# Performance work log

Measured on AMD Instinct MI355X. Metric: run time of the kernel, lower is better.

Reference implementation:

```python
import jax, jax.numpy as jnp
import numpy as np
from jax import lax

EPS = 1e-5
K = 32  # k_neighbor

def conv1(x, w):
    # x: [B, Cin, L], w: [Cout, Cin] (1x1 conv, no bias)
    return jnp.einsum('bcl,oc->bol', x, w)

def bn(x, g, b):
    # BatchNorm1d in training mode: batch statistics over (batch, length)
    m = jnp.mean(x, axis=(0, 2), keepdims=True)
    v = jnp.var(x, axis=(0, 2), keepdims=True)
    return g[None, :, None] * (x - m) / jnp.sqrt(v + EPS) + b[None, :, None]

def res_block(x, w1, g1, b1, w2, g2, b2):
    h = jax.nn.gelu(bn(conv1(x, w1), g1, b1), approximate=False)
    h = bn(conv1(h, w2), g2, b2)
    return jax.nn.gelu(h + x, approximate=False)

def extraction(x, conv_w, bn_g, bn_b, fw, fg, fb):
    # conv_w: [n_blocks, 2, C, C]; bn_g/bn_b: [n_blocks, 2, C]
    for i in range(conv_w.shape[0]):
        x = res_block(x, conv_w[i, 0], bn_g[i, 0], bn_b[i, 0],
                      conv_w[i, 1], bn_g[i, 1], bn_b[i, 1])
    # TransformerBlock: ffn (conv+BN) with residual + GELU
    return jax.nn.gelu(x + bn(conv1(x, fw), fg, fb), approximate=False)

def setup_inputs() -> dict:
    key = jax.random.key(0)
    ks = jax.random.split(key, 16)
    B, N, S, C = 8, 4096, 1024, 128  # C = out_channel = 2*channel
    inp = {
        'xyz': jax.random.normal(ks[0], (B, N, 3), dtype=jnp.float32),
        'x': jax.random.normal(ks[1], (B, 64, N), dtype=jnp.float32),
        'fps_idx': jax.random.randint(ks[2], (B, S), 0, N, dtype=jnp.int64),
        'pre_conv_w': jax.random.normal(ks[3], (2, 2, C, C), dtype=jnp.float32) * 0.05,
        'pre_bn_g': jnp.ones((2, 2, C), jnp.float32),
        'pre_bn_b': jnp.zeros((2, 2, C), jnp.float32),
        'pre_ffn_w': jax.random.normal(ks[4], (C, C), dtype=jnp.float32) * 0.05,
        'pre_ffn_g': jnp.ones((C,), jnp.float32),
        'pre_ffn_b': jnp.zeros((C,), jnp.float32),
        'pos_conv_w': jax.random.normal(ks[5], (2, 2, C, C), dtype=jnp.float32) * 0.05,
        'pos_bn_g': jnp.ones((2, 2, C), jnp.float32),
        'pos_bn_b': jnp.zeros((2, 2, C), jnp.float32),
        'pos_ffn_w': jax.random.normal(ks[6], (C, C), dtype=jnp.float32) * 0.05,
        'pos_ffn_g': jnp.ones((C,), jnp.float32),
        'pos_ffn_b': jnp.zeros((C,), jnp.float32),
    }
    return inp

def reference(xyz, x, fps_idx,
              pre_conv_w, pre_bn_g, pre_bn_b, pre_ffn_w, pre_ffn_g, pre_ffn_b,
              pos_conv_w, pos_bn_g, pos_bn_b, pos_ffn_w, pos_ffn_g, pos_ffn_b):
    B, N, _ = xyz.shape
    S = fps_idx.shape[1]
    points = jnp.swapaxes(x, 1, 2)  # [B, N, d]
    d = points.shape[-1]

    # --- LocalGrouper ---
    new_xyz = jnp.take_along_axis(xyz, fps_idx[:, :, None], axis=1)      # [B, S, 3]
    new_pts = jnp.take_along_axis(points, fps_idx[:, :, None], axis=1)  # [B, S, d]

    # squared distances [B, S, N]
    sqr = (jnp.sum(new_xyz ** 2, -1)[:, :, None]
           + jnp.sum(xyz ** 2, -1)[:, None, :]
           - 2.0 * jnp.einsum('bsc,bnc->bsn', new_xyz, xyz))
    idx = lax.top_k(-sqr, K)[1]  # [B, S, K] smallest distances

    grouped = jnp.take_along_axis(points, idx.reshape(B, S * K)[:, :, None],
                                  axis=1).reshape(B, S, K, d)
    center = new_pts[:, :, None, :]  # [B, S, 1, d]
    feat = jnp.concatenate([grouped - center,
                            jnp.broadcast_to(center, grouped.shape)], axis=-1)  # [B,S,K,2d]

    C = 2 * d
    # --- PreExtraction: [B,S,K,C] -> [B*S, C, K] -> maxpool -> [B, C, S] ---
    y = jnp.swapaxes(feat, 2, 3).reshape(B * S, C, K)
    y = extraction(y, pre_conv_w, pre_bn_g, pre_bn_b, pre_ffn_w, pre_ffn_g, pre_ffn_b)
    y = jnp.max(y, axis=-1).reshape(B, S, C)
    y = jnp.swapaxes(y, 1, 2)  # [B, C, S]

    # --- PosExtraction ---
    y = extraction(y, pos_conv_w, pos_bn_g, pos_bn_b, pos_ffn_w, pos_ffn_g, pos_ffn_b)
    return (new_xyz, y)
```

## Files before the change

kernel.cpp:

```cpp
#include <hip/hip_runtime.h>
#include <math.h>

typedef unsigned short ushort_t;
typedef unsigned long long u64;
typedef unsigned int uint32;

#define B_ 8
#define N_ 4096
#define S_ 1024
#define K_ 32
#define C_ 128
#define NCOL1 (B_*S_*K_)
#define NCOL2 (B_*S_)
#define EPS_ 1e-5f

typedef ushort_t us8 __attribute__((ext_vector_type(8)));
typedef short s16x8 __attribute__((ext_vector_type(8)));
typedef float f32x4 __attribute__((ext_vector_type(4)));

__device__ __forceinline__ float bf2f(ushort_t u){ return __uint_as_float(((uint32)u)<<16); }
__device__ __forceinline__ ushort_t f2bf(float f){
    uint32 x = __float_as_uint(f);
    return (ushort_t)((x + 0x7FFFu + ((x>>16)&1u)) >> 16);
}
__device__ __forceinline__ float gelu_f(float v){
    float az = fabsf(v)*0.70710678118654752f;
    float t  = __builtin_amdgcn_rcpf(fmaf(0.3275911f, az, 1.0f));
    float p  = fmaf(fmaf(fmaf(fmaf(1.061405429f, t, -1.453152027f), t, 1.421413741f), t,
                   -0.284496736f), t, 0.254829592f)*t;
    float e  = __expf(-az*az);
    float er = fmaf(-p, e, 1.0f);
    float s  = (v < 0.0f) ? -er : er;
    return 0.5f*v*(1.0f+s);
}
__device__ __forceinline__ u64 shfl_xor_u64(u64 v, int m){
    int lo = __shfl_xor((int)(v & 0xFFFFFFFFull), m, 64);
    int hi = __shfl_xor((int)(v >> 32), m, 64);
    return (((u64)(uint32)hi) << 32) | (uint32)lo;
}
__device__ __forceinline__ void gl_lds16(const char* gp, char* lp){
    __builtin_amdgcn_global_load_lds((const __attribute__((address_space(1))) void*)gp,
                                     (__attribute__((address_space(3))) void*)lp, 16, 0, 0);
}

__global__ __launch_bounds__(256) void transpose_kernel(const float* __restrict__ x, float* __restrict__ xT){
    __shared__ float t[64][65];
    int b  = blockIdx.x >> 6;
    int n0 = (blockIdx.x & 63) * 64;
    int tx = threadIdx.x & 63, ty = threadIdx.x >> 6;
    #pragma unroll
    for (int i=0;i<16;i++){
        int c = i*4 + ty;
        t[c][tx] = x[((long)(b*64 + c))*N_ + n0 + tx];
    }
    __syncthreads();
    #pragma unroll
    for (int i=0;i<16;i++){
        int n = i*4 + ty;
        xT[((long)(b*N_ + n0 + n))*64 + tx] = t[tx][n];
    }
}

__global__ __launch_bounds__(256) void knn_kernel(const float* __restrict__ xyz, const int* __restrict__ fps,
                                                  int* __restrict__ idxg, float* __restrict__ newxyz){
    __shared__ uint32 hist[4096];
    __shared__ u64    cand[1024];
    __shared__ u64    out_keys[64];
    __shared__ uint32 csum[256];
    __shared__ uint32 wtot[4];
    __shared__ uint32 shv[8];
    __shared__ u64    wred[4];
    __shared__ u64    winner;

    int tid = threadIdx.x;
    int wv = tid >> 6, l = tid & 63;
    int bs = blockIdx.x;
    int b  = bs >> 10;
    int qi = fps[bs];
    const float* qb = xyz + ((long)b*N_ + qi)*3;
    float qx = qb[0], qy = qb[1], qz = qb[2];
    if (tid < 3) newxyz[(long)bs*3 + tid] = qb[tid];
    const float* xb = xyz + (long)b*N_*3;

    for (int i=tid;i<1024;i+=256) hist[i]=0;
    if (tid < 8) shv[tid]=0;
    __syncthreads();

    uint32 dbits[16];
    #pragma unroll
    for (int i=0;i<16;i++){
        int n = i*256 + tid;
        float dx = xb[n*3+0]-qx, dy = xb[n*3+1]-qy, dz = xb[n*3+2]-qz;
        float d = dx*dx + dy*dy + dz*dz;
        dbits[i] = __float_as_uint(d);
        atomicAdd(&hist[dbits[i]>>21], 1u);
    }
    __syncthreads();

    {
        uint32 h4[4]; uint32 csumv=0;
        #pragma unroll
        for (int i=0;i<4;i++){ h4[i]=hist[tid*4+i]; csumv+=h4[i]; }
        uint32 sc = csumv;
        #pragma unroll
        for (int off=1; off<64; off<<=1){ uint32 o=__shfl_up(sc,off,64); if (l>=off) sc+=o; }
        if (l==63) wtot[wv]=sc;
        csum[tid]=sc;
        __syncthreads();
        uint32 base=0;
        for (int w2=0; w2<wv; w2++) base += wtot[w2];
        uint32 cum = base + csum[tid] - csumv;
        #pragma unroll
        for (int i=0;i<4;i++){
            if (cum <= 31u && 31u < cum + h4[i]){ shv[0]=(uint32)(tid*4+i); shv[1]=cum; }
            cum += h4[i];
        }
    }
    __syncthreads();
    uint32 b1 = shv[0], cl1 = shv[1];

    for (int i=tid;i<4096;i+=256) hist[i]=0;
    __syncthreads();
    #pragma unroll
    for (int i=0;i<16;i++){
        uint32 u = dbits[i];
        if ((u>>21)==b1) atomicAdd(&hist[(u>>9)&0xFFFu], 1u);
    }
    __syncthreads();

    uint32 r2 = 31u - cl1;
    {
        uint32 h[16]; uint32 csumv=0;
        #pragma unroll
        for (int i=0;i<16;i++){ h[i]=hist[tid*16+i]; csumv += h[i]; }
        uint32 sc = csumv;
        #pragma unroll
        for (int off=1; off<64; off<<=1){ uint32 o=__shfl_up(sc,off,64); if (l>=off) sc+=o; }
        if (l==63) wtot[wv]=sc;
        csum[tid]=sc;
        __syncthreads();
        uint32 base=0;
        for (int w2=0; w2<wv; w2++) base += wtot[w2];
        uint32 cum = base + csum[tid] - csumv;
        #pragma unroll
        for (int i=0;i<16;i++){
            if (cum <= r2 && r2 < cum + h[i]){ shv[2]=(uint32)(tid*16+i); shv[3]=cum; }
            cum += h[i];
        }
    }
    __syncthreads();
    uint32 b2 = shv[2], cl2 = shv[3];
    uint32 nless = cl1 + cl2;

    #pragma unroll
    for (int i=0;i<16;i++){
        uint32 u = dbits[i];
        int n = i*256 + tid;
        uint32 bb1 = u >> 21;
        if (bb1 > b1) continue;
        u64 key = (((u64)u)<<32) | (uint32)n;
        if (bb1 < b1){
            uint32 p = atomicAdd(&shv[4],1u); out_keys[p] = key;
        } else {
            uint32 bb2 = (u>>9)&0xFFFu;
            if (bb2 < b2){ uint32 p = atomicAdd(&shv[4],1u); out_keys[p] = key; }
            else if (bb2 == b2){ uint32 p = atomicAdd(&shv[5],1u); if (p < 1024u) cand[p] = key; }
        }
    }
    __syncthreads();

    if (shv[5] > 1024u){
        uint32 alive = 0xFFFFu;
        for (int r=0;r<K_;r++){
            u64 lmin = ~0ull;
            #pragma unroll
            for (int i=0;i<16;i++){
                u64 k = (((u64)dbits[i])<<32) | (uint32)(i*256+tid);
                if (((alive>>i)&1u) && k < lmin) lmin = k;
            }
            #pragma unroll
            for (int off=32; off>=1; off>>=1){
                u64 o = shfl_xor_u64(lmin, off);
                if (o < lmin) lmin = o;
            }
            if (l == 0) wred[wv] = lmin;
            __syncthreads();
            if (tid == 0){
                u64 m = wred[0];
                if (wred[1]<m) m=wred[1];
                if (wred[2]<m) m=wred[2];
                if (wred[3]<m) m=wred[3];
                winner = m;
                idxg[(long)bs*K_ + r] = (int)(m & 0xFFFFFFFFull);
            }
            __syncthreads();
            u64 w = winner;
            #pragma unroll
            for (int i=0;i<16;i++){
                u64 k = (((u64)dbits[i])<<32) | (uint32)(i*256+tid);
                if (k == w) alive &= ~(1u<<i);
            }
        }
    } else if (wv == 0){
        uint32 cb   = shv[5];
        uint32 need = 32u - nless;
        for (uint32 r=0; r<need; r++){
            u64 lmin = ~0ull;
            for (uint32 s=l; s<cb; s+=64){ u64 kk = cand[s]; if (kk < lmin) lmin = kk; }
            #pragma unroll
            for (int off=32; off>=1; off>>=1){
                u64 o = shfl_xor_u64(lmin, off);
                if (o < lmin) lmin = o;
            }
            for (uint32 s=l; s<cb; s+=64){ if (cand[s]==lmin) cand[s] = ~0ull; }
            if (l==0) out_keys[nless + r] = lmin;
        }
        u64 key = (l < 32) ? out_keys[l] : ~0ull;
        #pragma unroll
        for (uint32 k=2; k<=64; k<<=1){
            bool dir = ((l & k)==0);
            #pragma unroll
            for (uint32 j=k>>1; j>=1; j>>=1){
                u64 o = shfl_xor_u64(key, j);
                bool lower = ((l & j)==0);
                u64 mn = (key < o) ? key : o;
                u64 mx = (key < o) ? o : key;
                key = (lower == dir) ? mn : mx;
            }
        }
        if (l < 32) idxg[(long)bs*K_ + l] = (int)(key & 0xFFFFFFFFull);
    }
}

__global__ __launch_bounds__(256) void build_kernel(const float* __restrict__ xT, const int* __restrict__ fps,
                                                    const int* __restrict__ idxg, ushort_t* __restrict__ A){
    long col = (long)blockIdx.x*256 + threadIdx.x;
    long bs  = col >> 5;
    int  b   = (int)(bs >> 10);
    int  n   = idxg[col];
    int  cn  = fps[bs];
    const float4* pr = (const float4*)(xT + ((long)b*N_ + n )*64);
    const float4* cr = (const float4*)(xT + ((long)b*N_ + cn)*64);
    ushort_t* op = A + col*C_;
    #pragma unroll
    for (int j=0;j<16;j++){
        float4 p = pr[j], c = cr[j];
        uint2 d, e;
        d.x = (((uint32)f2bf(p.y-c.y))<<16) | f2bf(p.x-c.x);
        d.y = (((uint32)f2bf(p.w-c.w))<<16) | f2bf(p.z-c.z);
        e.x = (((uint32)f2bf(c.y))<<16) | f2bf(c.x);
        e.y = (((uint32)f2bf(c.w))<<16) | f2bf(c.z);
        *(uint2*)(op + j*4)      = d;
        *(uint2*)(op + 64 + j*4) = e;
    }
}

__global__ __launch_bounds__(256) void wcvt_kernel(const float* __restrict__ pcw, const float* __restrict__ pfw,
                                                   const float* __restrict__ qcw, const float* __restrict__ qfw,
                                                   ushort_t* __restrict__ Wb){
    int i = blockIdx.x*256 + threadIdx.x;
    int mat = i >> 14;
    int r = i & 16383;
    float v;
    if (mat < 4)      v = pcw[i];
    else if (mat == 4) v = pfw[r];
    else if (mat < 9)  v = qcw[i - 5*16384];
    else               v = qfw[r];
    Wb[i] = f2bf(v);
}

template<int MODE, int PROLOG>
__global__ __launch_bounds__(256) void conv_mfma(const ushort_t* in1, const ushort_t* in2, ushort_t* aux,
                                                 ushort_t* out, const ushort_t* __restrict__ Wb,
                                                 const float* __restrict__ scsh_g, const float* __restrict__ pbprev,
                                                 const float* __restrict__ g, const float* __restrict__ bb,
                                                 float* __restrict__ pb, int nb, float inv_cnt){
    __shared__ ushort_t inT[16384];
    __shared__ float ss[256];
    __shared__ float sL[4][128], qL[4][128];
    int tid = threadIdx.x;
    int w = tid >> 6, l = tid & 63;
    int l15 = l & 15, l4 = l >> 4;

    {
        const char* gt = (const char*)(in1 + (((long)blockIdx.x) << 7)*C_);
        char* lb = (char*)inT;
        #pragma unroll
        for (int i=0;i<8;i++){
            int p = i*4096 + w*1024 + l*16;
            int src = p ^ (((p>>8)&7)<<4);
            gl_lds16(gt + src, lb + i*4096 + w*1024);
        }
    }

    long col0 = ((long)blockIdx.x << 7) + ((long)w << 5);

    s16x8 a2[8];
    if (MODE == 2){
        #pragma unroll
        for (int t=0;t<8;t++){
            int n = t>>2, ks = t&3;
            a2[t] = *(const s16x8*)(in2 + (col0 + n*16 + l15)*C_ + ks*32 + l4*8);
        }
    }

    if (MODE > 0){
        if (PROLOG){
            if (tid < 128){
                const float4* ps = (const float4*)(pbprev + tid*64);
                const float4* pq = (const float4*)(pbprev + (128+tid)*64);
                float s=0.f, q=0.f;
                #pragma unroll
                for (int i=0;i<16;i++){ float4 a=ps[i]; s += (a.x+a.y)+(a.z+a.w); }
                #pragma unroll
                for (int i=0;i<16;i++){ float4 a=pq[i]; q += (a.x+a.y)+(a.z+a.w); }
                float mean = s*inv_cnt, var = q*inv_cnt - mean*mean;
                float sc = g[tid]*rsqrtf(var+EPS_);
                ss[tid*2]   = sc;
                ss[tid*2+1] = bb[tid] - mean*sc;
            }
        } else {
            ss[tid] = scsh_g[tid];
        }
    }
    __syncthreads();

    const char* lb = (const char*)inT;
    f32x4 acc[8][2] = {};
    #pragma unroll
    for (int ks=0; ks<4; ks++){
        int kl = ks*32 + l4*8;
        s16x8 af[8];
        #pragma unroll
        for (int m=0;m<8;m++)
            af[m] = *(const s16x8*)(Wb + (m*16 + l15)*C_ + kl);
        s16x8 bv[2];
        #pragma unroll
        for (int n=0;n<2;n++){
            int colr = (w<<5) + n*16 + l15;
            int boff = (ks*64 + l4*16) ^ ((l15&7)<<4);
            bv[n] = *(const s16x8*)(lb + colr*256 + boff);
        }
        if (MODE > 0){
            float sc[8], sh[8];
            const float4* sp = (const float4*)(&ss[kl*2]);
            float4 s0 = sp[0], s1 = sp[1], s2 = sp[2], s3 = sp[3];
            sc[0]=s0.x; sh[0]=s0.y; sc[1]=s0.z; sh[1]=s0.w;
            sc[2]=s1.x; sh[2]=s1.y; sc[3]=s1.z; sh[3]=s1.w;
            sc[4]=s2.x; sh[4]=s2.y; sc[5]=s2.z; sh[5]=s2.w;
            sc[6]=s3.x; sh[6]=s3.y; sc[7]=s3.z; sh[7]=s3.w;
            #pragma unroll
            for (int n=0;n<2;n++){
                s16x8 v = bv[n];
                if (MODE == 1){
                    #pragma unroll
                    for (int e=0;e<8;e++){
                        float f = gelu_f(fmaf(bf2f((ushort_t)v[e]), sc[e], sh[e]));
                        v[e] = (short)f2bf(f);
                    }
                } else {
                    s16x8 a = a2[n*4+ks];
                    #pragma unroll
                    for (int e=0;e<8;e++){
                        float f = gelu_f(fmaf(bf2f((ushort_t)v[e]), sc[e], sh[e]) + bf2f((ushort_t)a[e]));
                        v[e] = (short)f2bf(f);
                    }
                }
                bv[n] = v;
                if (MODE == 2)
                    *(s16x8*)(aux + (col0 + n*16 + l15)*C_ + kl) = v;
            }
        }
        #pragma unroll
        for (int m=0;m<8;m++)
            #pragma unroll
            for (int n=0;n<2;n++)
                acc[m][n] = __builtin_amdgcn_mfma_f32_16x16x32_bf16(af[m], bv[n], acc[m][n], 0, 0, 0);
    }

    #pragma unroll
    for (int n=0;n<2;n++){
        long cadr = (col0 + n*16 + l15)*C_;
        #pragma unroll
        for (int m=0;m<8;m++){
            f32x4 a = acc[m][n];
            uint2 st;
            st.x = (((uint32)f2bf(a[1]))<<16) | f2bf(a[0]);
            st.y = (((uint32)f2bf(a[3]))<<16) | f2bf(a[2]);
            *(uint2*)(out + cadr + m*16 + l4*4) = st;
        }
    }

    #pragma unroll
    for (int m=0;m<8;m++){
        #pragma unroll
        for (int r=0;r<4;r++){
            float a0=acc[m][0][r], a1=acc[m][1][r];
            float s = a0+a1;
            float q = a0*a0+a1*a1;
            #pragma unroll
            for (int off=1; off<16; off<<=1){
                s += __shfl_xor(s, off, 64);
                q += __shfl_xor(q, off, 64);
            }
            if (l15 == 0){
                sL[w][m*16 + l4*4 + r] = s;
                qL[w][m*16 + l4*4 + r] = q;
            }
        }
    }
    __syncthreads();
    if (tid < 128){
        float s = sL[0][tid] + sL[1][tid] + sL[2][tid] + sL[3][tid];
        float q = qL[0][tid] + qL[1][tid] + qL[2][tid] + qL[3][tid];
        pb[(long)tid*nb + blockIdx.x]       = s;
        pb[(long)(128+tid)*nb + blockIdx.x] = q;
    }
}

__global__ __launch_bounds__(256) void reduce_fin_kernel(const float* __restrict__ pb, float* __restrict__ scsh,
                                                         const float* __restrict__ g, const float* __restrict__ bb,
                                                         float inv_cnt, int nb){
    int oc = blockIdx.x;
    float s=0.f, q=0.f;
    for (int b=threadIdx.x; b<nb; b+=256){
        s += pb[(long)oc*nb + b];
        q += pb[(long)(128+oc)*nb + b];
    }
    __shared__ float ls[256], lq[256];
    ls[threadIdx.x]=s; lq[threadIdx.x]=q;
    __syncthreads();
    #pragma unroll
    for (int st_=128; st_>0; st_>>=1){
        if (threadIdx.x < st_){ ls[threadIdx.x]+=ls[threadIdx.x+st_]; lq[threadIdx.x]+=lq[threadIdx.x+st_]; }
        __syncthreads();
    }
    if (threadIdx.x==0){
        float mean = ls[0]*inv_cnt;
        float var  = lq[0]*inv_cnt - mean*mean;
        float sc   = g[oc]*rsqrtf(var + EPS_);
        scsh[oc*2+0] = sc;
        scsh[oc*2+1] = bb[oc] - mean*sc;
    }
}

__global__ __launch_bounds__(256) void pool_kernel(const ushort_t* __restrict__ T, const ushort_t* __restrict__ X,
                                                   const float* __restrict__ scsh, ushort_t* __restrict__ A2){
    long p  = (long)blockIdx.x*256 + threadIdx.x;
    long bs = p >> 6;
    int  c0 = ((int)p & 63)*2;
    float sc0=scsh[c0*2], sh0=scsh[c0*2+1], sc1=scsh[c0*2+2], sh1=scsh[c0*2+3];
    const ushort_t* tb = T + (bs*K_)*(long)C_ + c0;
    const ushort_t* xv = X + (bs*K_)*(long)C_ + c0;
    float m0 = -1e30f, m1 = -1e30f;
    #pragma unroll 4
    for (int k=0;k<K_;k++){
        uint32 tv = *(const uint32*)(tb + (long)k*C_);
        uint32 av = *(const uint32*)(xv + (long)k*C_);
        float v0 = gelu_f(fmaf(bf2f((ushort_t)(tv & 0xFFFFu)), sc0, sh0) + bf2f((ushort_t)(av & 0xFFFFu)));
        float v1 = gelu_f(fmaf(bf2f((ushort_t)(tv >> 16)),     sc1, sh1) + bf2f((ushort_t)(av >> 16)));
        m0 = fmaxf(m0, v0);
        m1 = fmaxf(m1, v1);
    }
    uint32 o = (((uint32)f2bf(m1))<<16) | f2bf(m0);
    *(uint32*)(A2 + bs*C_ + c0) = o;
}

__global__ __launch_bounds__(256) void out_kernel(const ushort_t* __restrict__ T, const ushort_t* __restrict__ X,
                                                  const float* __restrict__ scsh, float* __restrict__ y){
    long o = (long)blockIdx.x*256 + threadIdx.x;
    int s = (int)(o & (S_-1));
    int c = (int)((o >> 10) & (C_-1));
    int b = (int)(o >> 17);
    long ad = ((long)(b*S_ + s))*C_ + c;
    float v = gelu_f(fmaf(bf2f(T[ad]), scsh[c*2], scsh[c*2+1]) + bf2f(X[ad]));
    y[o] = v;
}

extern "C" void kernel_launch(void* const* d_in, const int* in_sizes, int n_in,
                              void* d_out, int out_size, void* d_ws, size_t ws_size,
                              hipStream_t stream){
    const float* xyz        = (const float*)d_in[0];
    const float* x          = (const float*)d_in[1];
    const int*   fps        = (const int*)d_in[2];
    const float* pre_bn_g   = (const float*)d_in[4];
    const float* pre_bn_b   = (const float*)d_in[5];
    const float* pre_ffn_g  = (const float*)d_in[7];
    const float* pre_ffn_b  = (const float*)d_in[8];
    const float* pos_bn_g   = (const float*)d_in[10];
    const float* pos_bn_b   = (const float*)d_in[11];
    const float* pos_ffn_g  = (const float*)d_in[13];
    const float* pos_ffn_b  = (const float*)d_in[14];

    float* out_xyz = (float*)d_out;
    float* out_y   = (float*)d_out + (long)B_*S_*3;

    char* ws = (char*)d_ws;
    float*    scsh  = (float*)(ws + 0);
    float*    pb2a  = (float*)(ws + 10240);
    float*    pb2b  = (float*)(ws + 75776);
    ushort_t* Wb    = (ushort_t*)(ws + 141312);
    int*      idx   = (int*)(ws + 468992);
    float*    pb    = (float*)(ws + 468992);
    float*    xT    = (float*)(ws + 2566144);
    ushort_t* A2    = (ushort_t*)(ws + 2566144);
    ushort_t* C2    = (ushort_t*)(ws + 4663296);
    ushort_t* A1    = (ushort_t*)(ws + 10954752);
    ushort_t* Cb    = (ushort_t*)(ws + 78063616);
    (void)in_sizes; (void)n_in; (void)out_size; (void)ws_size;

    const float inv1 = 1.0f/(float)NCOL1, inv2 = 1.0f/(float)NCOL2;
    const ushort_t* Wp = Wb;
    const ushort_t* Wq = Wb + 5*C_*C_;

    wcvt_kernel<<<640,256,0,stream>>>((const float*)d_in[3], (const float*)d_in[6],
                                      (const float*)d_in[9], (const float*)d_in[12], Wb);
    transpose_kernel<<<B_*(N_/64),256,0,stream>>>(x, xT);
    knn_kernel<<<B_*S_,256,0,stream>>>(xyz, fps, idx, out_xyz);
    build_kernel<<<NCOL1/256,256,0,stream>>>(xT, fps, idx, A1);

    {
        int nb = NCOL1/128;
        const float* G[5]  = {pre_bn_g, pre_bn_g+C_, pre_bn_g+2*C_, pre_bn_g+3*C_, pre_ffn_g};
        const float* Bv[5] = {pre_bn_b, pre_bn_b+C_, pre_bn_b+2*C_, pre_bn_b+3*C_, pre_ffn_b};
        conv_mfma<0,0><<<nb,256,0,stream>>>(A1, nullptr, nullptr, Cb, Wp+0*C_*C_, nullptr, nullptr, nullptr, nullptr, pb, nb, inv1);
        reduce_fin_kernel<<<128,256,0,stream>>>(pb, scsh+0*256, G[0], Bv[0], inv1, nb);
        conv_mfma<1,0><<<nb,256,0,stream>>>(Cb, nullptr, nullptr, Cb, Wp+1*C_*C_, scsh+0*256, nullptr, nullptr, nullptr, pb, nb, inv1);
        reduce_fin_kernel<<<128,256,0,stream>>>(pb, scsh+1*256, G[1], Bv[1], inv1, nb);
        conv_mfma<2,0><<<nb,256,0,stream>>>(Cb, A1, A1, Cb, Wp+2*C_*C_, scsh+1*256, nullptr, nullptr, nullptr, pb, nb, inv1);
        reduce_fin_kernel<<<128,256,0,stream>>>(pb, scsh+2*256, G[2], Bv[2], inv1, nb);
        conv_mfma<1,0><<<nb,256,0,stream>>>(Cb, nullptr, nullptr, Cb, Wp+3*C_*C_, scsh+2*256, nullptr, nullptr, nullptr, pb, nb, inv1);
        reduce_fin_kernel<<<128,256,0,stream>>>(pb, scsh+3*256, G[3], Bv[3], inv1, nb);
        conv_mfma<2,0><<<nb,256,0,stream>>>(Cb, A1, A1, Cb, Wp+4*C_*C_, scsh+3*256, nullptr, nullptr, nullptr, pb, nb, inv1);
        reduce_fin_kernel<<<128,256,0,stream>>>(pb, scsh+4*256, G[4], Bv[4], inv1, nb);
        pool_kernel<<<(NCOL2*64)/256,256,0,stream>>>(Cb, A1, scsh+4*256, A2);
    }

    {
        int nb = NCOL2/128;
        const float* G[5]  = {pos_bn_g, pos_bn_g+C_, pos_bn_g+2*C_, pos_bn_g+3*C_, pos_ffn_g};
        const float* Bv[5] = {pos_bn_b, pos_bn_b+C_, pos_bn_b+2*C_, pos_bn_b+3*C_, pos_ffn_b};
        conv_mfma<0,1><<<nb,256,0,stream>>>(A2, nullptr, nullptr, C2, Wq+0*C_*C_, nullptr, nullptr, nullptr, nullptr, pb2a, nb, inv2);
        conv_mfma<1,1><<<nb,256,0,stream>>>(C2, nullptr, nullptr, C2, Wq+1*C_*C_, nullptr, pb2a, G[0], Bv[0], pb2b, nb, inv2);
        conv_mfma<2,1><<<nb,256,0,stream>>>(C2, A2, A2, C2, Wq+2*C_*C_, nullptr, pb2b, G[1], Bv[1], pb2a, nb, inv2);
        conv_mfma<1,1><<<nb,256,0,stream>>>(C2, nullptr, nullptr, C2, Wq+3*C_*C_, nullptr, pb2a, G[2], Bv[2], pb2b, nb, inv2);
        conv_mfma<2,1><<<nb,256,0,stream>>>(C2, A2, A2, C2, Wq+4*C_*C_, nullptr, pb2b, G[3], Bv[3], pb2a, nb, inv2);
        reduce_fin_kernel<<<128,256,0,stream>>>(pb2a, scsh+5*256, G[4], Bv[4], inv2, nb);
        out_kernel<<<(B_*C_*S_)/256,256,0,stream>>>(C2, A2, scsh+5*256, out_y);
    }
}
```

Baseline: 665.5 us.

## Factor first grouped conv into per-point U/V GEMMs and fuse pos-extraction into one kernel

The first 1x1 conv over the grouped features is split algebraically: W·[p-c; c] = W_lo·p + (W_hi-W_lo)·c. U is computed per input point and V per centre, then gathered and added, so the materialised A1 feature tensor and its GEMM are no longer needed. The residual input for the second block is rebuilt on the fly from bf16 transposed points instead of being read from A1. The whole PosExtraction stage runs in a single 64-block persistent kernel that uses atomic-counter grid barriers for the BN statistics, replacing several launches and the separate output kernel. The costs are extra rounding from bf16 U/V, a different order of bf16 rounding, and reliance on all 64 blocks being resident at once for the spin barrier.

```diff
diff --git a/kernel.cpp b/kernel.cpp
--- a/kernel.cpp
+++ b/kernel.cpp
@@ -43,7 +43,7 @@
                                      (__attribute__((address_space(3))) void*)lp, 16, 0, 0);
 }
 
-__global__ __launch_bounds__(256) void transpose_kernel(const float* __restrict__ x, float* __restrict__ xT){
+__global__ __launch_bounds__(256) void transpose_kernel(const float* __restrict__ x, ushort_t* __restrict__ xTb){
     __shared__ float t[64][65];
     int b  = blockIdx.x >> 6;
     int n0 = (blockIdx.x & 63) * 64;
@@ -57,7 +57,7 @@
     #pragma unroll
     for (int i=0;i<16;i++){
         int n = i*4 + ty;
-        xT[((long)(b*N_ + n0 + n))*64 + tx] = t[tx][n];
+        xTb[((long)(b*N_ + n0 + n))*64 + tx] = f2bf(t[tx][n]);
     }
 }
 
@@ -232,48 +232,86 @@
     }
 }
 
-__global__ __launch_bounds__(256) void build_kernel(const float* __restrict__ xT, const int* __restrict__ fps,
-                                                    const int* __restrict__ idxg, ushort_t* __restrict__ A){
-    long col = (long)blockIdx.x*256 + threadIdx.x;
-    long bs  = col >> 5;
-    int  b   = (int)(bs >> 10);
-    int  n   = idxg[col];
-    int  cn  = fps[bs];
-    const float4* pr = (const float4*)(xT + ((long)b*N_ + n )*64);
-    const float4* cr = (const float4*)(xT + ((long)b*N_ + cn)*64);
-    ushort_t* op = A + col*C_;
-    #pragma unroll
-    for (int j=0;j<16;j++){
-        float4 p = pr[j], c = cr[j];
-        uint2 d, e;
-        d.x = (((uint32)f2bf(p.y-c.y))<<16) | f2bf(p.x-c.x);
-        d.y = (((uint32)f2bf(p.w-c.w))<<16) | f2bf(p.z-c.z);
-        e.x = (((uint32)f2bf(c.y))<<16) | f2bf(c.x);
-        e.y = (((uint32)f2bf(c.w))<<16) | f2bf(c.z);
-        *(uint2*)(op + j*4)      = d;
-        *(uint2*)(op + 64 + j*4) = e;
-    }
-}
-
 __global__ __launch_bounds__(256) void wcvt_kernel(const float* __restrict__ pcw, const float* __restrict__ pfw,
                                                    const float* __restrict__ qcw, const float* __restrict__ qfw,
-                                                   ushort_t* __restrict__ Wb){
+                                                   ushort_t* __restrict__ Wb, ushort_t* __restrict__ UW,
+                                                   ushort_t* __restrict__ VW){
     int i = blockIdx.x*256 + threadIdx.x;
-    int mat = i >> 14;
-    int r = i & 16383;
-    float v;
-    if (mat < 4)      v = pcw[i];
-    else if (mat == 4) v = pfw[r];
-    else if (mat < 9)  v = qcw[i - 5*16384];
-    else               v = qfw[r];
-    Wb[i] = f2bf(v);
-}
-
-template<int MODE, int PROLOG>
+    if (i < 163840){
+        int mat = i >> 14;
+        int r = i & 16383;
+        float v;
+        if (mat < 4)       v = pcw[i];
+        else if (mat == 4) v = pfw[r];
+        else if (mat < 9)  v = qcw[i - 5*16384];
+        else               v = qfw[r];
+        Wb[i] = f2bf(v);
+    } else {
+        int j = i - 163840;
+        int jj = j & 8191;
+        int oc = jj >> 6, c = jj & 63;
+        if (j < 8192) UW[jj] = f2bf(pcw[oc*128 + c]);
+        else          VW[jj] = f2bf(pcw[oc*128 + 64 + c] - pcw[oc*128 + c]);
+    }
+}
+
+__global__ __launch_bounds__(256) void uv_gemm(const ushort_t* __restrict__ xTb, const int* __restrict__ fps,
+                                               const ushort_t* __restrict__ UW, const ushort_t* __restrict__ VW,
+                                               ushort_t* __restrict__ U, ushort_t* __restrict__ V2){
+    int tid = threadIdx.x;
+    int w = tid >> 6, l = tid & 63;
+    int l15 = l & 15, l4 = l >> 4;
+    bool isV = blockIdx.x >= 256;
+    int base = (isV ? (int)(blockIdx.x - 256) : (int)blockIdx.x)*128 + w*32;
+    const ushort_t* Wh = isV ? VW : UW;
+    ushort_t* out = isV ? V2 : U;
+
+    long xrow[2];
+    #pragma unroll
+    for (int n=0;n<2;n++){
+        int r = base + n*16 + l15;
+        if (isV){ int b = r >> 10; xrow[n] = ((long)(b<<12) + fps[r]); }
+        else    { xrow[n] = r; }
+    }
+    f32x4 acc[8][2] = {};
+    #pragma unroll
+    for (int ks=0; ks<2; ks++){
+        int kl = ks*32 + l4*8;
+        s16x8 af[8];
+        #pragma unroll
+        for (int m=0;m<8;m++)
+            af[m] = *(const s16x8*)(Wh + (m*16 + l15)*64 + kl);
+        s16x8 bv[2];
+        #pragma unroll
+        for (int n=0;n<2;n++)
+            bv[n] = *(const s16x8*)(xTb + xrow[n]*64 + kl);
+        #pragma unroll
+        for (int m=0;m<8;m++)
+            #pragma unroll
+            for (int n=0;n<2;n++)
+                acc[m][n] = __builtin_amdgcn_mfma_f32_16x16x32_bf16(af[m], bv[n], acc[m][n], 0, 0, 0);
+    }
+    #pragma unroll
+    for (int n=0;n<2;n++){
+        long radr = (long)(base + n*16 + l15)*C_;
+        #pragma unroll
+        for (int m=0;m<8;m++){
+            f32x4 a = acc[m][n];
+            uint2 st;
+            st.x = (((uint32)f2bf(a[1]))<<16) | f2bf(a[0]);
+            st.y = (((uint32)f2bf(a[3]))<<16) | f2bf(a[2]);
+            *(uint2*)(out + radr + m*16 + l4*4) = st;
+        }
+    }
+}
+
+template<int MODE>
 __global__ __launch_bounds__(256) void conv_mfma(const ushort_t* in1, const ushort_t* in2, ushort_t* aux,
                                                  ushort_t* out, const ushort_t* __restrict__ Wb,
-                                                 const float* __restrict__ scsh_g, const float* __restrict__ pbprev,
-                                                 const float* __restrict__ g, const float* __restrict__ bb,
+                                                 const float* __restrict__ scsh_g,
+                                                 const ushort_t* __restrict__ U, const ushort_t* __restrict__ V2,
+                                                 const ushort_t* __restrict__ xTb, const int* __restrict__ idxg,
+                                                 const int* __restrict__ fps,
                                                  float* __restrict__ pb, int nb, float inv_cnt){
     __shared__ ushort_t inT[16384];
     __shared__ float ss[256];
@@ -281,8 +319,9 @@
     int tid = threadIdx.x;
     int w = tid >> 6, l = tid & 63;
     int l15 = l & 15, l4 = l >> 4;
-
-    {
+    long col0 = ((long)blockIdx.x << 7) + ((long)w << 5);
+
+    if (MODE != 3){
         const char* gt = (const char*)(in1 + (((long)blockIdx.x) << 7)*C_);
         char* lb = (char*)inT;
         #pragma unroll
@@ -293,8 +332,6 @@
         }
     }
 
-    long col0 = ((long)blockIdx.x << 7) + ((long)w << 5);
-
     s16x8 a2[8];
     if (MODE == 2){
         #pragma unroll
@@ -303,79 +340,103 @@
             a2[t] = *(const s16x8*)(in2 + (col0 + n*16 + l15)*C_ + ks*32 + l4*8);
         }
     }
-
-    if (MODE > 0){
-        if (PROLOG){
-            if (tid < 128){
-                const float4* ps = (const float4*)(pbprev + tid*64);
-                const float4* pq = (const float4*)(pbprev + (128+tid)*64);
-                float s=0.f, q=0.f;
+    if (MODE == 4){
+        int bs = (int)(col0 >> 5);
+        int b  = bs >> 10;
+        int cc = fps[bs];
+        const ushort_t* crow = xTb + ((long)(b<<12) + cc)*64;
+        s16x8 c0 = *(const s16x8*)(crow + l4*8);
+        s16x8 c1 = *(const s16x8*)(crow + 32 + l4*8);
+        #pragma unroll
+        for (int n=0;n<2;n++){
+            int nn = idxg[col0 + n*16 + l15];
+            const ushort_t* prow = xTb + ((long)(b<<12) + nn)*64;
+            s16x8 p0 = *(const s16x8*)(prow + l4*8);
+            s16x8 p1 = *(const s16x8*)(prow + 32 + l4*8);
+            s16x8 d0, d1;
+            #pragma unroll
+            for (int e=0;e<8;e++){
+                d0[e] = (short)f2bf(bf2f((ushort_t)p0[e]) - bf2f((ushort_t)c0[e]));
+                d1[e] = (short)f2bf(bf2f((ushort_t)p1[e]) - bf2f((ushort_t)c1[e]));
+            }
+            a2[n*4+0] = d0; a2[n*4+1] = d1; a2[n*4+2] = c0; a2[n*4+3] = c1;
+        }
+    }
+    if (MODE == 1 || MODE == 2 || MODE == 4) ss[tid] = scsh_g[tid];
+    __syncthreads();
+
+    f32x4 acc[8][2] = {};
+    if (MODE == 3){
+        int bs = (int)(col0 >> 5);
+        int b  = bs >> 10;
+        const ushort_t* vrow = V2 + (long)bs*C_;
+        #pragma unroll
+        for (int n=0;n<2;n++){
+            int nn = idxg[col0 + n*16 + l15];
+            const ushort_t* urow = U + ((long)(b*4096) + nn)*C_;
+            #pragma unroll
+            for (int m=0;m<8;m++){
+                int oc0 = m*16 + l4*4;
+                uint2 uu = *(const uint2*)(urow + oc0);
+                uint2 vv = *(const uint2*)(vrow + oc0);
+                acc[m][n][0] = bf2f((ushort_t)(uu.x & 0xFFFFu)) + bf2f((ushort_t)(vv.x & 0xFFFFu));
+                acc[m][n][1] = bf2f((ushort_t)(uu.x >> 16))     + bf2f((ushort_t)(vv.x >> 16));
+                acc[m][n][2] = bf2f((ushort_t)(uu.y & 0xFFFFu)) + bf2f((ushort_t)(vv.y & 0xFFFFu));
+                acc[m][n][3] = bf2f((ushort_t)(uu.y >> 16))     + bf2f((ushort_t)(vv.y >> 16));
+            }
+        }
+    } else {
+        const char* lb = (const char*)inT;
+        #pragma unroll
+        for (int ks=0; ks<4; ks++){
+            int kl = ks*32 + l4*8;
+            s16x8 af[8];
+            #pragma unroll
+            for (int m=0;m<8;m++)
+                af[m] = *(const s16x8*)(Wb + (m*16 + l15)*C_ + kl);
+            s16x8 bv[2];
+            #pragma unroll
+            for (int n=0;n<2;n++){
+                int colr = (w<<5) + n*16 + l15;
+                int boff = (ks*64 + l4*16) ^ ((l15&7)<<4);
+                bv[n] = *(const s16x8*)(lb + colr*256 + boff);
+            }
+            {
+                float sc[8], sh[8];
+                const float4* sp = (const float4*)(&ss[kl*2]);
+                float4 s0 = sp[0], s1 = sp[1], s2 = sp[2], s3 = sp[3];
+                sc[0]=s0.x; sh[0]=s0.y; sc[1]=s0.z; sh[1]=s0.w;
+                sc[2]=s1.x; sh[2]=s1.y; sc[3]=s1.z; sh[3]=s1.w;
+                sc[4]=s2.x; sh[4]=s2.y; sc[5]=s2.z; sh[5]=s2.w;
+                sc[6]=s3.x; sh[6]=s3.y; sc[7]=s3.z; sh[7]=s3.w;
                 #pragma unroll
-                for (int i=0;i<16;i++){ float4 a=ps[i]; s += (a.x+a.y)+(a.z+a.w); }
+                for (int n=0;n<2;n++){
+                    s16x8 v = bv[n];
+                    if (MODE == 1){
+                        #pragma unroll
+                        for (int e=0;e<8;e++){
+                            float f = gelu_f(fmaf(bf2f((ushort_t)v[e]), sc[e], sh[e]));
+                            v[e] = (short)f2bf(f);
+                        }
+                    } else {
+                        s16x8 a = a2[n*4+ks];
+                        #pragma unroll
+                        for (int e=0;e<8;e++){
+                            float f = gelu_f(fmaf(bf2f((ushort_t)v[e]), sc[e], sh[e]) + bf2f((ushort_t)a[e]));
+                            v[e] = (short)f2bf(f);
+                        }
+                    }
+                    bv[n] = v;
+                    if (MODE == 2 || MODE == 4)
+                        *(s16x8*)(aux + (col0 + n*16 + l15)*C_ + kl) = v;
+                }
+            }
+            #pragma unroll
+            for (int m=0;m<8;m++)
                 #pragma unroll
-                for (int i=0;i<16;i++){ float4 a=pq[i]; q += (a.x+a.y)+(a.z+a.w); }
-                float mean = s*inv_cnt, var = q*inv_cnt - mean*mean;
-                float sc = g[tid]*rsqrtf(var+EPS_);
-                ss[tid*2]   = sc;
-                ss[tid*2+1] = bb[tid] - mean*sc;
-            }
-        } else {
-            ss[tid] = scsh_g[tid];
-        }
-    }
-    __syncthreads();
-
-    const char* lb = (const char*)inT;
-    f32x4 acc[8][2] = {};
-    #pragma unroll
-    for (int ks=0; ks<4; ks++){
-        int kl = ks*32 + l4*8;
-        s16x8 af[8];
-        #pragma unroll
-        for (int m=0;m<8;m++)
-            af[m] = *(const s16x8*)(Wb + (m*16 + l15)*C_ + kl);
-        s16x8 bv[2];
-        #pragma unroll
-        for (int n=0;n<2;n++){
-            int colr = (w<<5) + n*16 + l15;
-            int boff = (ks*64 + l4*16) ^ ((l15&7)<<4);
-            bv[n] = *(const s16x8*)(lb + colr*256 + boff);
-        }
-        if (MODE > 0){
-            float sc[8], sh[8];
-            const float4* sp = (const float4*)(&ss[kl*2]);
-            float4 s0 = sp[0], s1 = sp[1], s2 = sp[2], s3 = sp[3];
-            sc[0]=s0.x; sh[0]=s0.y; sc[1]=s0.z; sh[1]=s0.w;
-            sc[2]=s1.x; sh[2]=s1.y; sc[3]=s1.z; sh[3]=s1.w;
-            sc[4]=s2.x; sh[4]=s2.y; sc[5]=s2.z; sh[5]=s2.w;
-            sc[6]=s3.x; sh[6]=s3.y; sc[7]=s3.z; sh[7]=s3.w;
-            #pragma unroll
-            for (int n=0;n<2;n++){
-                s16x8 v = bv[n];
-                if (MODE == 1){
-                    #pragma unroll
-                    for (int e=0;e<8;e++){
-                        float f = gelu_f(fmaf(bf2f((ushort_t)v[e]), sc[e], sh[e]));
-                        v[e] = (short)f2bf(f);
-                    }
-                } else {
-                    s16x8 a = a2[n*4+ks];
-                    #pragma unroll
-                    for (int e=0;e<8;e++){
-                        float f = gelu_f(fmaf(bf2f((ushort_t)v[e]), sc[e], sh[e]) + bf2f((ushort_t)a[e]));
-                        v[e] = (short)f2bf(f);
-                    }
-                }
-                bv[n] = v;
-                if (MODE == 2)
-                    *(s16x8*)(aux + (col0 + n*16 + l15)*C_ + kl) = v;
-            }
-        }
-        #pragma unroll
-        for (int m=0;m<8;m++)
-            #pragma unroll
-            for (int n=0;n<2;n++)
-                acc[m][n] = __builtin_amdgcn_mfma_f32_16x16x32_bf16(af[m], bv[n], acc[m][n], 0, 0, 0);
+                for (int n=0;n<2;n++)
+                    acc[m][n] = __builtin_amdgcn_mfma_f32_16x16x32_bf16(af[m], bv[n], acc[m][n], 0, 0, 0);
+        }
     }
 
     #pragma unroll
@@ -466,15 +527,159 @@
     *(uint32*)(A2 + bs*C_ + c0) = o;
 }
 
-__global__ __launch_bounds__(256) void out_kernel(const ushort_t* __restrict__ T, const ushort_t* __restrict__ X,
-                                                  const float* __restrict__ scsh, float* __restrict__ y){
-    long o = (long)blockIdx.x*256 + threadIdx.x;
-    int s = (int)(o & (S_-1));
-    int c = (int)((o >> 10) & (C_-1));
-    int b = (int)(o >> 17);
-    long ad = ((long)(b*S_ + s))*C_ + c;
-    float v = gelu_f(fmaf(bf2f(T[ad]), scsh[c*2], scsh[c*2+1]) + bf2f(X[ad]));
-    y[o] = v;
+__device__ __forceinline__ void gbar(uint32* cnt, uint32 target){
+    __threadfence();
+    __syncthreads();
+    if (threadIdx.x == 0){
+        atomicAdd(cnt, 1u);
+        while (atomicAdd(cnt, 0u) < target){ __builtin_amdgcn_s_sleep(8); }
+    }
+    __syncthreads();
+    __threadfence();
+}
+
+template<int M>
+__device__ __forceinline__ void e2_phase(ushort_t* Ts, ushort_t* Xs, const ushort_t* Wp,
+                                         const float* ss, int w, int l15, int l4,
+                                         f32x4 (&acc)[8][2]){
+    char* tb = (char*)Ts;
+    char* xb = (char*)Xs;
+    const char* src = (M==0) ? (const char*)xb : (const char*)tb;
+    #pragma unroll
+    for (int ks=0; ks<4; ks++){
+        int kl = ks*32 + l4*8;
+        s16x8 af[8];
+        #pragma unroll
+        for (int m=0;m<8;m++)
+            af[m] = *(const s16x8*)(Wp + (m*16 + l15)*C_ + kl);
+        #pragma unroll
+        for (int n=0;n<2;n++){
+            int q  = (w*32 + n*16 + l15)*256 + ks*64 + l4*16;
+            int qs = q ^ (((q>>8)&7)<<4);
+            s16x8 v = *(const s16x8*)(src + qs);
+            if (M >= 1){
+                const float4* sp = (const float4*)(&ss[kl*2]);
+                float4 s0=sp[0], s1=sp[1], s2=sp[2], s3=sp[3];
+                float sc[8] = {s0.x,s0.z,s1.x,s1.z,s2.x,s2.z,s3.x,s3.z};
+                float sh[8] = {s0.y,s0.w,s1.y,s1.w,s2.y,s2.w,s3.y,s3.w};
+                s16x8 xv;
+                if (M == 2) xv = *(const s16x8*)(xb + qs);
+                #pragma unroll
+                for (int e=0;e<8;e++){
+                    float f = fmaf(bf2f((ushort_t)v[e]), sc[e], sh[e]);
+                    if (M == 2) f += bf2f((ushort_t)xv[e]);
+                    f = gelu_f(f);
+                    v[e] = (short)f2bf(f);
+                }
+                if (M == 2) *(s16x8*)(xb + qs) = v;
+            }
+            #pragma unroll
+            for (int m=0;m<8;m++)
+                acc[m][n] = __builtin_amdgcn_mfma_f32_16x16x32_bf16(af[m], v, acc[m][n], 0, 0, 0);
+        }
+    }
+    asm volatile("s_waitcnt lgkmcnt(0)" ::: "memory");
+    __builtin_amdgcn_sched_barrier(0);
+    #pragma unroll
+    for (int n=0;n<2;n++){
+        #pragma unroll
+        for (int m=0;m<8;m++){
+            f32x4 a = acc[m][n];
+            uint2 st;
+            st.x = (((uint32)f2bf(a[1]))<<16) | f2bf(a[0]);
+            st.y = (((uint32)f2bf(a[3]))<<16) | f2bf(a[2]);
+            int q2  = (w*32 + n*16 + l15)*256 + (m*16 + l4*4)*2;
+            int qs2 = q2 ^ (((q2>>8)&7)<<4);
+            *(uint2*)(tb + qs2) = st;
+        }
+    }
+}
+
+__global__ __launch_bounds__(256) void ext2_kernel(const ushort_t* __restrict__ A2, const ushort_t* __restrict__ Wq,
+        const float* __restrict__ bng, const float* __restrict__ bnb,
+        const float* __restrict__ fg, const float* __restrict__ fb,
+        float* __restrict__ pbE, uint32* cnt, float* __restrict__ y, float inv_cnt){
+    __shared__ ushort_t Ts[16384];
+    __shared__ ushort_t Xs[16384];
+    __shared__ float ss[256];
+    __shared__ float sL[4][128], qL[4][128];
+    int tid = threadIdx.x, w = tid>>6, l = tid&63, l15 = l&15, l4 = l>>4;
+    int blk = blockIdx.x;
+
+    {
+        const char* gt = (const char*)(A2 + ((long)blk << 7)*C_);
+        #pragma unroll
+        for (int i=0;i<8;i++){
+            int p = i*4096 + w*1024 + l*16;
+            int src = p ^ (((p>>8)&7)<<4);
+            gl_lds16(gt + src, (char*)Xs + i*4096 + w*1024);
+        }
+    }
+    __syncthreads();
+
+    #pragma unroll
+    for (int ph=0; ph<5; ph++){
+        f32x4 acc[8][2] = {};
+        if      (ph==0) e2_phase<0>(Ts, Xs, Wq + 0*C_*C_, ss, w, l15, l4, acc);
+        else if (ph==1) e2_phase<1>(Ts, Xs, Wq + 1*C_*C_, ss, w, l15, l4, acc);
+        else if (ph==2) e2_phase<2>(Ts, Xs, Wq + 2*C_*C_, ss, w, l15, l4, acc);
+        else if (ph==3) e2_phase<1>(Ts, Xs, Wq + 3*C_*C_, ss, w, l15, l4, acc);
+        else            e2_phase<2>(Ts, Xs, Wq + 4*C_*C_, ss, w, l15, l4, acc);
+
+        #pragma unroll
+        for (int m=0;m<8;m++){
+            #pragma unroll
+            for (int r=0;r<4;r++){
+                float a0=acc[m][0][r], a1=acc[m][1][r];
+                float s=a0+a1, q=a0*a0+a1*a1;
+                #pragma unroll
+                for (int off=1; off<16; off<<=1){
+                    s += __shfl_xor(s, off, 64);
+                    q += __shfl_xor(q, off, 64);
+                }
+                if (l15 == 0){ sL[w][m*16+l4*4+r]=s; qL[w][m*16+l4*4+r]=q; }
+            }
+        }
+        __syncthreads();
+        float* pbS = pbE + ph*16384;
+        if (tid < 128){
+            float s = sL[0][tid]+sL[1][tid]+sL[2][tid]+sL[3][tid];
+            float q = qL[0][tid]+qL[1][tid]+qL[2][tid]+qL[3][tid];
+            pbS[tid*64 + blk]       = s;
+            pbS[(128+tid)*64 + blk] = q;
+        }
+        gbar(cnt, 64u*(uint32)(ph+1));
+        if (tid < 128){
+            float s=0.f, q=0.f;
+            #pragma unroll 8
+            for (int k=0;k<64;k++){ s += pbS[tid*64+k]; q += pbS[(128+tid)*64+k]; }
+            float mean = s*inv_cnt, var = q*inv_cnt - mean*mean;
+            float gg = (ph<4) ? bng[ph*128 + tid] : fg[tid];
+            float bv = (ph<4) ? bnb[ph*128 + tid] : fb[tid];
+            float sc = gg*rsqrtf(var + EPS_);
+            ss[tid*2]   = sc;
+            ss[tid*2+1] = bv - mean*sc;
+        }
+        __syncthreads();
+    }
+
+    int b  = blk >> 3;
+    int s0 = (blk & 7) * 128;
+    int colL = tid & 127;
+    int rep  = tid >> 7;
+    #pragma unroll
+    for (int cb=0; cb<8; cb++){
+        int q  = colL*256 + rep*128 + cb*16;
+        int qs = q ^ (((q>>8)&7)<<4);
+        s16x8 tvv = *(const s16x8*)((char*)Ts + qs);
+        s16x8 xvv = *(const s16x8*)((char*)Xs + qs);
+        #pragma unroll
+        for (int e=0;e<8;e++){
+            int c = rep*64 + cb*8 + e;
+            float f = gelu_f(fmaf(bf2f((ushort_t)tvv[e]), ss[c*2], ss[c*2+1]) + bf2f((ushort_t)xvv[e]));
+            y[((long)(b*C_ + c))*S_ + s0 + colL] = f;
+        }
+    }
 }
 
 extern "C" void kernel_launch(void* const* d_in, const int* in_sizes, int n_in,
@@ -483,12 +688,16 @@
     const float* xyz        = (const float*)d_in[0];
     const float* x          = (const float*)d_in[1];
     const int*   fps        = (const int*)d_in[2];
+    const float* pre_conv_w = (const float*)d_in[3];
     const float* pre_bn_g   = (const float*)d_in[4];
     const float* pre_bn_b   = (const float*)d_in[5];
+    const float* pre_ffn_w  = (const float*)d_in[6];
     const float* pre_ffn_g  = (const float*)d_in[7];
     const float* pre_ffn_b  = (const float*)d_in[8];
+    const float* pos_conv_w = (const float*)d_in[9];
     const float* pos_bn_g   = (const float*)d_in[10];
     const float* pos_bn_b   = (const float*)d_in[11];
+    const float* pos_ffn_w  = (const float*)d_in[12];
     const float* pos_ffn_g  = (const float*)d_in[13];
     const float* pos_ffn_b  = (const float*)d_in[14];
 
@@ -496,56 +705,54 @@
     float* out_y   = (float*)d_out + (long)B_*S_*3;
 
     char* ws = (char*)d_ws;
-    float*    scsh  = (float*)(ws + 0);
-    float*    pb2a  = (float*)(ws + 10240);
-    float*    pb2b  = (float*)(ws + 75776);
-    ushort_t* Wb    = (ushort_t*)(ws + 141312);
-    int*      idx   = (int*)(ws + 468992);
-    float*    pb    = (float*)(ws + 468992);
-    float*    xT    = (float*)(ws + 2566144);
-    ushort_t* A2    = (ushort_t*)(ws + 2566144);
-    ushort_t* C2    = (ushort_t*)(ws + 4663296);
-    ushort_t* A1    = (ushort_t*)(ws + 10954752);
-    ushort_t* Cb    = (ushort_t*)(ws + 78063616);
+    float*    scsh = (float*)(ws + 0);
+    uint32*   cnt  = (uint32*)(ws + 8192);
+    float*    pbE  = (float*)(ws + 10240);
+    ushort_t* Wb   = (ushort_t*)(ws + 337920);
+    ushort_t* UW   = (ushort_t*)(ws + 665600);
+    ushort_t* VW   = (ushort_t*)(ws + 681984);
+    int*      idx  = (int*)(ws + 698368);
+    ushort_t* xTb  = (ushort_t*)(ws + 1746944);
+    ushort_t* A2   = (ushort_t*)(ws + 5941248);
+    float*    pb1  = (float*)(ws + 8038400);
+    ushort_t* Cb   = (ushort_t*)(ws + 10135552);
+    ushort_t* X    = (ushort_t*)(ws + 77244416);
+    ushort_t* U    = (ushort_t*)(ws + 77244416);
+    ushort_t* V2   = (ushort_t*)(ws + 85633024);
     (void)in_sizes; (void)n_in; (void)out_size; (void)ws_size;
 
     const float inv1 = 1.0f/(float)NCOL1, inv2 = 1.0f/(float)NCOL2;
     const ushort_t* Wp = Wb;
     const ushort_t* Wq = Wb + 5*C_*C_;
-
-    wcvt_kernel<<<640,256,0,stream>>>((const float*)d_in[3], (const float*)d_in[6],
-                                      (const float*)d_in[9], (const float*)d_in[12], Wb);
-    transpose_kernel<<<B_*(N_/64),256,0,stream>>>(x, xT);
+    const int nb = 2048;
+
+    hipMemsetAsync(cnt, 0, 64, stream);
+    wcvt_kernel<<<704,256,0,stream>>>(pre_conv_w, pre_ffn_w, pos_conv_w, pos_ffn_w, Wb, UW, VW);
+    transpose_kernel<<<B_*(N_/64),256,0,stream>>>(x, xTb);
     knn_kernel<<<B_*S_,256,0,stream>>>(xyz, fps, idx, out_xyz);
-    build_kernel<<<NCOL1/256,256,0,stream>>>(xT, fps, idx, A1);
+    uv_gemm<<<320,256,0,stream>>>(xTb, fps, UW, VW, U, V2);
 
     {
-        int nb = NCOL1/128;
         const float* G[5]  = {pre_bn_g, pre_bn_g+C_, pre_bn_g+2*C_, pre_bn_g+3*C_, pre_ffn_g};
         const float* Bv[5] = {pre_bn_b, pre_bn_b+C_, pre_bn_b+2*C_, pre_bn_b+3*C_, pre_ffn_b};
-        conv_mfma<0,0><<<nb,256,0,stream>>>(A1, nullptr, nullptr, Cb, Wp+0*C_*C_, nullptr, nullptr, nullptr, nullptr, pb, nb, inv1);
-        reduce_fin_kernel<<<128,256,0,stream>>>(pb, scsh+0*256, G[0], Bv[0], inv1, nb);
-        conv_mfma<1,0><<<nb,256,0,stream>>>(Cb, nullptr, nullptr, Cb, Wp+1*C_*C_, scsh+0*256, nullptr, nullptr, nullptr, pb, nb, inv1);
-        reduce_fin_kernel<<<128,256,0,stream>>>(pb, scsh+1*256, G[1], Bv[1], inv1, nb);
-        conv_mfma<2,0><<<nb,256,0,stream>>>(Cb, A1, A1, Cb, Wp+2*C_*C_, scsh+1*256, nullptr, nullptr, nullptr, pb, nb, inv1);
-        reduce_fin_kernel<<<128,256,0,stream>>>(pb, scsh+2*256, G[2], Bv[2], inv1, nb);
-        conv_mfma<1,0><<<nb,256,0,stream>>>(Cb, nullptr, nullptr, Cb, Wp+3*C_*C_, scsh+2*256, nullptr, nullptr, nullptr, pb, nb, inv1);
-        reduce_fin_kernel<<<128,256,0,stream>>>(pb, scsh+3*256, G[3], Bv[3], inv1, nb);
-        conv_mfma<2,0><<<nb,256,0,stream>>>(Cb, A1, A1, Cb, Wp+4*C_*C_, scsh+3*256, nullptr, nullptr, nullptr, pb, nb, inv1);
-        reduce_fin_kernel<<<128,256,0,stream>>>(pb, scsh+4*256, G[4], Bv[4], inv1, nb);
-        pool_kernel<<<(NCOL2*64)/256,256,0,stream>>>(Cb, A1, scsh+4*256, A2);
-    }
-
-    {
-        int nb = NCOL2/128;
-        const float* G[5]  = {pos_bn_g, pos_bn_g+C_, pos_bn_g+2*C_, pos_bn_g+3*C_, pos_ffn_g};
-        const float* Bv[5] = {pos_bn_b, pos_bn_b+C_, pos_bn_b+2*C_, pos_bn_b+3*C_, pos_ffn_b};
-        conv_mfma<0,1><<<nb,256,0,stream>>>(A2, nullptr, nullptr, C2, Wq+0*C_*C_, nullptr, nullptr, nullptr, nullptr, pb2a, nb, inv2);
-        conv_mfma<1,1><<<nb,256,0,stream>>>(C2, nullptr, nullptr, C2, Wq+1*C_*C_, nullptr, pb2a, G[0], Bv[0], pb2b, nb, inv2);
-        conv_mfma<2,1><<<nb,256,0,stream>>>(C2, A2, A2, C2, Wq+2*C_*C_, nullptr, pb2b, G[1], Bv[1], pb2a, nb, inv2);
-        conv_mfma<1,1><<<nb,256,0,stream>>>(C2, nullptr, nullptr, C2, Wq+3*C_*C_, nullptr, pb2a, G[2], Bv[2], pb2b, nb, inv2);
-        conv_mfma<2,1><<<nb,256,0,stream>>>(C2, A2, A2, C2, Wq+4*C_*C_, nullptr, pb2b, G[3], Bv[3], pb2a, nb, inv2);
-        reduce_fin_kernel<<<128,256,0,stream>>>(pb2a, scsh+5*256, G[4], Bv[4], inv2, nb);
-        out_kernel<<<(B_*C_*S_)/256,256,0,stream>>>(C2, A2, scsh+5*256, out_y);
-    }
-}
+        conv_mfma<3><<<nb,256,0,stream>>>(nullptr, nullptr, nullptr, Cb, nullptr, nullptr,
+                                          U, V2, nullptr, idx, fps, pb1, nb, inv1);
+        reduce_fin_kernel<<<128,256,0,stream>>>(pb1, scsh+0*256, G[0], Bv[0], inv1, nb);
+        conv_mfma<1><<<nb,256,0,stream>>>(Cb, nullptr, nullptr, Cb, Wp+1*C_*C_, scsh+0*256,
+                                          nullptr, nullptr, nullptr, nullptr, nullptr, pb1, nb, inv1);
+        reduce_fin_kernel<<<128,256,0,stream>>>(pb1, scsh+1*256, G[1], Bv[1], inv1, nb);
+        conv_mfma<4><<<nb,256,0,stream>>>(Cb, nullptr, X, Cb, Wp+2*C_*C_, scsh+1*256,
+                                          nullptr, nullptr, xTb, idx, fps, pb1, nb, inv1);
+        reduce_fin_kernel<<<128,256,0,stream>>>(pb1, scsh+2*256, G[2], Bv[2], inv1, nb);
+        conv_mfma<1><<<nb,256,0,stream>>>(Cb, nullptr, nullptr, Cb, Wp+3*C_*C_, scsh+2*256,
+                                          nullptr, nullptr, nullptr, nullptr, nullptr, pb1, nb, inv1);
+        reduce_fin_kernel<<<128,256,0,stream>>>(pb1, scsh+3*256, G[3], Bv[3], inv1, nb);
+        conv_mfma<2><<<nb,256,0,stream>>>(Cb, X, X, Cb, Wp+4*C_*C_, scsh+3*256,
+                                          nullptr, nullptr, nullptr, nullptr, nullptr, pb1, nb, inv1);
+        reduce_fin_kernel<<<128,256,0,stream>>>(pb1, scsh+4*256, G[4], Bv[4], inv1, nb);
+        pool_kernel<<<(NCOL2*64)/256,256,0,stream>>>(Cb, X, scsh+4*256, A2);
+    }
+
+    ext2_kernel<<<64,256,0,stream>>>(A2, Wq, pos_bn_g, pos_bn_b, pos_ffn_g, pos_ffn_b,
+                                     pbE, cnt, out_y, inv2);
+}
```

Result: faster. 648.5 us (-2.6%).
